# Kernel optimization log

Measured on AMD Instinct MI355X. Metric: run time of the kernel, lower is better.

The kernel has to match this reference:

```python
import jax, jax.numpy as jnp
import numpy as np

N, D, K, P, A = 16384, 256, 32, 64, 5
H, KD, NPT, FACT = 8, 32, 8, 2
RBF_BINS, RBF_MAX, REL_CLIP = 16, 10.0, 32


def _norm(v, eps=1e-6):
    return v * jax.lax.rsqrt(jnp.square(v).sum(-1, keepdims=True) + eps)


def extract_frames(pos):
    # pos: [N, A, 3]; backbone atoms 0=N, 1=CA, 2=C (Gram-Schmidt AF-style frame)
    n, ca, c = pos[:, 0], pos[:, 1], pos[:, 2]
    e1 = _norm(c - ca)
    u = n - ca
    e2 = _norm(u - (u * e1).sum(-1, keepdims=True) * e1)
    e3 = jnp.cross(e1, e2)
    R = jnp.stack([e1, e2, e3], axis=-1)  # [N,3,3], columns = frame axes
    t = ca
    local = jnp.einsum('nji,naj->nai', R, pos - t[:, None])  # R^T (p - t)
    return R, t, local


def distance_rbf(d):
    centers = jnp.linspace(0.0, RBF_MAX, RBF_BINS)
    sigma = RBF_MAX / RBF_BINS
    return jnp.exp(-jnp.square((d[..., None] - centers) / sigma))


def layer_norm(x, scale, offset, eps=1e-5):
    mu = x.mean(-1, keepdims=True)
    var = jnp.square(x - mu).mean(-1, keepdims=True)
    return (x - mu) * jax.lax.rsqrt(var + eps) * scale + offset


def setup_inputs() -> dict:
    key = jax.random.key(0)
    ks = jax.random.split(key, 20)
    f32 = jnp.float32
    rnd = lambda i, shape, s=0.02: jax.random.normal(ks[i], shape, f32) * s
    inp = {}
    inp['local'] = jax.random.normal(ks[0], (N, D), f32)
    inp['pos'] = jax.random.normal(ks[1], (N, A, 3), f32) * 3.0
    inp['neighbours'] = jax.random.randint(ks[2], (N, K), 0, N, jnp.int32)
    inp['resi'] = jnp.arange(N, dtype=jnp.int32) % 512
    inp['chain'] = jnp.arange(N, dtype=jnp.int32) // 2048
    inp['batch'] = jnp.arange(N, dtype=jnp.int32) // 4096
    inp['update_mask'] = jnp.ones((N, 1), bool)
    inp['mask'] = jnp.ones((N,), bool)
    FIN = A * 3 + A * RBF_BINS
    FPAIR = A * 3 + A * RBF_BINS + (2 * REL_CLIP + 1) + 2
    FOUT = H * KD + H * P + H * NPT * 3 + H * NPT
    inp['w_in'] = rnd(3, (FIN, D))
    inp['w_pair'] = rnd(4, (FPAIR, P))
    inp['b_pair'] = jnp.zeros((P,), f32)
    inp['ln1_s'] = jnp.ones((D,), f32); inp['ln1_o'] = jnp.zeros((D,), f32)
    inp['wq'] = rnd(5, (D, H * KD)); inp['wk'] = rnd(6, (D, H * KD)); inp['wv'] = rnd(7, (D, H * KD))
    inp['wqp'] = rnd(8, (D, H * NPT * 3)); inp['wkp'] = rnd(9, (D, H * NPT * 3)); inp['wvp'] = rnd(10, (D, H * NPT * 3))
    inp['wb'] = rnd(11, (P, H))
    inp['gamma'] = jnp.ones((H,), f32)
    inp['wo'] = rnd(12, (FOUT, D)); inp['bo'] = jnp.zeros((D,), f32)
    inp['ln2_s'] = jnp.ones((D,), f32); inp['ln2_o'] = jnp.zeros((D,), f32)
    DH = D * FACT
    inp['wg'] = rnd(13, (D, DH)); inp['wvm'] = rnd(14, (D, DH)); inp['wom'] = rnd(15, (DH, D))
    inp['ln3_s'] = jnp.ones((D,), f32); inp['ln3_o'] = jnp.zeros((D,), f32)
    inp['wpos'] = rnd(16, (D, A * 3))
    return inp


def reference(local, pos, w_in, w_pair, b_pair, ln1_s, ln1_o, wq, wk, wv, wqp, wkp, wvp,
              wb, gamma, wo, bo, ln2_s, ln2_o, wg, wvm, wom, ln3_s, ln3_o, wpos,
              neighbours, resi, chain, batch, update_mask, mask):
    n_res = local.shape[0]
    kk = neighbours.shape[1]
    R, t, local_pos = extract_frames(pos)  # [N,3,3], [N,3], [N,A,3]
    # --- geometric input features ---
    dloc = jnp.sqrt(jnp.square(local_pos).sum(-1) + 1e-12)
    feat = jnp.concatenate([_norm(local_pos).reshape(n_res, -1),
                            distance_rbf(dloc).reshape(n_res, -1)], axis=-1)
    local = local + feat @ w_in
    # --- pair features over kNN edges ---
    idx = jnp.clip(neighbours, 0, n_res - 1)
    pos_j = pos[idx]  # [N,K,A,3]
    rel = jnp.einsum('nji,nkaj->nkai', R, pos_j - t[:, None, None])  # neighbour atoms in frame i
    dij = jnp.sqrt(jnp.square(rel).sum(-1) + 1e-12)  # [N,K,A]
    dirs = rel / (dij[..., None] + 1e-6)
    rp = jnp.clip(resi[idx] - resi[:, None], -REL_CLIP, REL_CLIP) + REL_CLIP
    rp_oh = jax.nn.one_hot(rp, 2 * REL_CLIP + 1, dtype=local.dtype)
    same_chain = (chain[idx] == chain[:, None])[..., None].astype(local.dtype)
    same_batch = (batch[idx] == batch[:, None])[..., None].astype(local.dtype)
    pf = jnp.concatenate([dirs.reshape(n_res, kk, -1), distance_rbf(dij).reshape(n_res, kk, -1),
                          rp_oh, same_chain, same_batch], axis=-1)
    pair = jax.nn.gelu(pf @ w_pair + b_pair)  # [N,K,P]
    pair_mask = mask[:, None] & mask[idx] & (neighbours >= 0) & (batch[idx] == batch[:, None])
    # --- sparse invariant point attention ---
    x = layer_norm(local, ln1_s, ln1_o)
    q = (x @ wq).reshape(n_res, H, KD)
    k = (x @ wk).reshape(n_res, H, KD)
    v = (x @ wv).reshape(n_res, H, KD)
    to_glob = lambda pts: jnp.einsum('nij,nhpj->nhpi', R, pts) + t[:, None, None]
    qp = to_glob((x @ wqp).reshape(n_res, H, NPT, 3))
    kp = to_glob((x @ wkp).reshape(n_res, H, NPT, 3))
    vp = to_glob((x @ wvp).reshape(n_res, H, NPT, 3))
    qk = jnp.einsum('nhd,nkhd->nkh', q, k[idx]) / np.float32(np.sqrt(KD))
    d2 = jnp.square(qp[:, None] - kp[idx]).sum(-1).sum(-1)  # [N,K,H]
    wc = np.float32(np.sqrt(2.0 / (9.0 * NPT)))
    wl = np.float32(np.sqrt(1.0 / 3.0))
    logits = wl * (qk + pair @ wb - 0.5 * wc * jax.nn.softplus(gamma) * d2)
    logits = jnp.where(pair_mask[..., None], logits, -1e9)
    att = jax.nn.softmax(logits, axis=1)
    att = jnp.where(pair_mask[..., None], att, 0.0)
    o_s = jnp.einsum('nkh,nkhd->nhd', att, v[idx]).reshape(n_res, -1)
    o_pt = jnp.einsum('nkh,nkhpi->nhpi', att, vp[idx])
    o_pt = jnp.einsum('nji,nhpj->nhpi', R, o_pt - t[:, None, None])  # back to local frame
    o_n = jnp.sqrt(jnp.square(o_pt).sum(-1) + 1e-8)
    o_pr = jnp.einsum('nkh,nkc->nhc', att, pair).reshape(n_res, -1)
    ipa = jnp.concatenate([o_s, o_pr, o_pt.reshape(n_res, -1), o_n.reshape(n_res, -1)], -1) @ wo + bo
    local = local + ipa
    # --- gated MLP ---
    x = layer_norm(local, ln2_s, ln2_o)
    local = local + (jax.nn.gelu(x @ wg) * (x @ wvm)) @ wom
    # --- equivariant position update (scale = 1.0) ---
    x = layer_norm(local, ln3_s, ln3_o)
    new_lp = local_pos + (x @ wpos).reshape(n_res, A, 3)
    new_pos = jnp.einsum('nij,naj->nai', R, new_lp) + t[:, None]
    pos = jnp.where(update_mask[..., None], new_pos, pos)
    return local, pos
```

## Files before the change

kernel.cpp:

```cpp
#include <hip/hip_runtime.h>
#include <hip/hip_bf16.h>
#include <math.h>

#define DMODEL 256
#define KNB 32
#define NHEAD 8
#define FIN 95
#define FPD 95
#define KPAD 104
#define FOUT 1024
#define DHID 512
#define BTS 36
#define PRS 72

typedef __hip_bfloat16 bf16;
typedef __attribute__((ext_vector_type(8))) short short8;
typedef __attribute__((ext_vector_type(4))) float floatx4;

__device__ inline float B2F(bf16 x) { return __bfloat162float(x); }
__device__ inline bf16 F2B(float x) { return __float2bfloat16(x); }
__device__ inline unsigned short f2bs(float x) {
    bf16 h = __float2bfloat16(x);
    return *reinterpret_cast<unsigned short*>(&h);
}
__device__ inline float bs2f(short s) {
    return __uint_as_float(((unsigned)(unsigned short)s) << 16);
}

__device__ inline float gelu_f(float x) {
    float u = 1.5957691216057308f * x * (1.f + 0.044715f * x * x);
    float t = 1.f - 2.f / (1.f + __expf(u));
    return 0.5f * x * (1.f + t);
}

#define OFF_WALL 0
#define OFF_WO   344064
#define OFF_WG   606208
#define OFF_WVM  737280
#define OFF_WOM  868352
#define OFF_WP   999424
#define OFF_WIN  1006080
#define OFF_WBM  1032704
#define WT_TOTAL 1033728

__global__ __launch_bounds__(256) void kT(const float* __restrict__ wq, const float* __restrict__ wk,
                                          const float* __restrict__ wv, const float* __restrict__ wqp,
                                          const float* __restrict__ wkp, const float* __restrict__ wvp,
                                          const float* __restrict__ wo, const float* __restrict__ wg,
                                          const float* __restrict__ wvm, const float* __restrict__ wom,
                                          const float* __restrict__ w_pair, const float* __restrict__ w_in,
                                          const float* __restrict__ wbm,
                                          unsigned short* __restrict__ wt) {
    int stride = gridDim.x * 256;
    for (int e = blockIdx.x * 256 + threadIdx.x; e < WT_TOTAL; e += stride) {
        float v;
        if (e < OFF_WO) {
            int n = e >> 8, k = e & 255;
            if (n < 256) v = wq[k * 256 + n];
            else if (n < 512) v = wk[k * 256 + n - 256];
            else if (n < 768) v = wv[k * 256 + n - 512];
            else if (n < 960) v = wqp[k * 192 + n - 768];
            else if (n < 1152) v = wkp[k * 192 + n - 960];
            else v = wvp[k * 192 + n - 1152];
        } else if (e < OFF_WG) {
            int u = e - OFF_WO; int n = u >> 10, k = u & 1023;
            v = wo[k * 256 + n];
        } else if (e < OFF_WVM) {
            int u = e - OFF_WG; int n = u >> 8, k = u & 255;
            v = wg[k * 512 + n];
        } else if (e < OFF_WOM) {
            int u = e - OFF_WVM; int n = u >> 8, k = u & 255;
            v = wvm[k * 512 + n];
        } else if (e < OFF_WP) {
            int u = e - OFF_WOM; int n = u >> 9, k = u & 511;
            v = wom[k * 256 + n];
        } else if (e < OFF_WIN) {
            int u = e - OFF_WP; int n = u / KPAD, k = u % KPAD;
            v = (k < FPD) ? w_pair[k * 64 + n] : 0.f;
        } else if (e < OFF_WBM) {
            int u = e - OFF_WIN; int n = u / KPAD, k = u % KPAD;
            v = (k < FIN) ? w_in[k * 256 + n] : 0.f;
        } else {
            int u = e - OFF_WBM; int n = u >> 6, k = u & 63;
            v = (n < NHEAD) ? wbm[k * 8 + n] : 0.f;
        }
        wt[e] = f2bs(v);
    }
}

__global__ __launch_bounds__(256) void kA1(const float* __restrict__ pos,
                                           float* __restrict__ Rw,
                                           float* __restrict__ lpw,
                                           unsigned short* __restrict__ featb) {
    int tid = threadIdx.x;
    int res = tid >> 5, lt = tid & 31;
    int ri = blockIdx.x * 8 + res;
    const float* pp = pos + (size_t)ri * 15;
    float nx = pp[0], ny = pp[1], nz = pp[2];
    float cax = pp[3], cay = pp[4], caz = pp[5];
    float cx = pp[6], cy = pp[7], cz = pp[8];
    float e1x = cx - cax, e1y = cy - cay, e1z = cz - caz;
    float inv = rsqrtf(e1x * e1x + e1y * e1y + e1z * e1z + 1e-6f);
    e1x *= inv; e1y *= inv; e1z *= inv;
    float ux = nx - cax, uy = ny - cay, uz = nz - caz;
    float d = ux * e1x + uy * e1y + uz * e1z;
    float wx = ux - d * e1x, wy = uy - d * e1y, wz = uz - d * e1z;
    inv = rsqrtf(wx * wx + wy * wy + wz * wz + 1e-6f);
    float e2x = wx * inv, e2y = wy * inv, e2z = wz * inv;
    float e3x = e1y * e2z - e1z * e2y;
    float e3y = e1z * e2x - e1x * e2z;
    float e3z = e1x * e2y - e1y * e2x;
    float R[9] = {e1x, e2x, e3x, e1y, e2y, e3y, e1z, e2z, e3z};

    __shared__ float lpS[8][15];
    __shared__ float ddS[8][5], dinvS[8][5];

    if (lt < 9) Rw[(size_t)ri * 9 + lt] = R[lt];
    if (lt < 15) {
        int a = lt / 3, ii = lt % 3;
        float px = pp[a * 3 + 0] - cax, py = pp[a * 3 + 1] - cay, pz = pp[a * 3 + 2] - caz;
        float v = R[0 * 3 + ii] * px + R[1 * 3 + ii] * py + R[2 * 3 + ii] * pz;
        lpS[res][lt] = v;
        lpw[(size_t)ri * 15 + lt] = v;
    }
    __syncthreads();
    if (lt < 5) {
        float s = lpS[res][lt * 3] * lpS[res][lt * 3] + lpS[res][lt * 3 + 1] * lpS[res][lt * 3 + 1] +
                  lpS[res][lt * 3 + 2] * lpS[res][lt * 3 + 2];
        ddS[res][lt] = sqrtf(s + 1e-12f);
        dinvS[res][lt] = rsqrtf(s + 1e-6f);
    }
    __syncthreads();
    for (int e = lt; e < KPAD; e += 32) {
        float v;
        if (e < 15) v = lpS[res][e] * dinvS[res][e / 3];
        else if (e < 95) {
            int u = e - 15, a = u >> 4, b = u & 15;
            float z = (ddS[res][a] - (float)b * (10.f / 15.f)) * (1.f / 0.625f);
            v = __expf(-z * z);
        } else v = 0.f;
        featb[(size_t)ri * KPAD + e] = f2bs(v);
    }
}

__global__ __launch_bounds__(256) void kB(const float* __restrict__ local,
                                          const unsigned short* __restrict__ featb,
                                          const float* __restrict__ ln1_s,
                                          const float* __restrict__ ln1_o,
                                          const unsigned short* __restrict__ wAllT,
                                          const unsigned short* __restrict__ w_inT,
                                          float* __restrict__ dlocal,
                                          bf16* __restrict__ qbh, bf16* __restrict__ kvb,
                                          bf16* __restrict__ qpl, bf16* __restrict__ kpl,
                                          bf16* __restrict__ vpl) {
    int r0 = blockIdx.x * 32;
    int tid = threadIdx.x;
    __shared__ __align__(16) unsigned short featA[32 * KPAD];
    __shared__ __align__(16) unsigned short xbf[32 * 264];
    __shared__ float statsS[32 * 4];

    {
        const short8* src = reinterpret_cast<const short8*>(featb + (size_t)r0 * KPAD);
        short8* dst = reinterpret_cast<short8*>(featA);
        for (int c = tid; c < 32 * KPAD / 8; c += 256) dst[c] = src[c];
    }
    __syncthreads();

    int lane = tid & 63, w = tid >> 6;
    int mtile = w & 1, par = w >> 1;
    int m = lane & 15, quad = lane >> 4;

    short8 fa[3];
#pragma unroll
    for (int ks = 0; ks < 3; ks++)
        fa[ks] = *reinterpret_cast<const short8*>(&featA[(mtile * 16 + m) * KPAD + ks * 32 + quad * 8]);
    float lupv[8][4];
#pragma unroll
    for (int j = 0; j < 8; j++) {
        int nt = par + 2 * j;
        floatx4 c = {0.f, 0.f, 0.f, 0.f};
        const short8* bp = reinterpret_cast<const short8*>(w_inT + (size_t)(nt * 16 + m) * KPAD);
#pragma unroll
        for (int ks = 0; ks < 3; ks++)
            c = __builtin_amdgcn_mfma_f32_16x16x32_bf16(fa[ks], bp[ks * 4 + quad], c, 0, 0, 0);
        int col = nt * 16 + m;
#pragma unroll
        for (int r = 0; r < 4; r++) {
            int row = mtile * 16 + quad * 4 + r;
            float lv = local[(size_t)(r0 + row) * 256 + col] + c[r];
            lupv[j][r] = lv;
            dlocal[(size_t)(r0 + row) * 256 + col] = lv;
        }
    }
    {
        float s[4] = {0.f, 0.f, 0.f, 0.f}, ss[4] = {0.f, 0.f, 0.f, 0.f};
#pragma unroll
        for (int j = 0; j < 8; j++)
#pragma unroll
            for (int r = 0; r < 4; r++) { s[r] += lupv[j][r]; ss[r] += lupv[j][r] * lupv[j][r]; }
#pragma unroll
        for (int mask = 1; mask < 16; mask <<= 1)
#pragma unroll
            for (int r = 0; r < 4; r++) { s[r] += __shfl_xor(s[r], mask); ss[r] += __shfl_xor(ss[r], mask); }
        if (m == 0) {
#pragma unroll
            for (int r = 0; r < 4; r++) {
                int row = mtile * 16 + quad * 4 + r;
                statsS[row * 4 + par * 2 + 0] = s[r];
                statsS[row * 4 + par * 2 + 1] = ss[r];
            }
        }
    }
    __syncthreads();
    {
        float mu[4], rs_[4];
#pragma unroll
        for (int r = 0; r < 4; r++) {
            int row = mtile * 16 + quad * 4 + r;
            float S = statsS[row * 4 + 0] + statsS[row * 4 + 2];
            float SS = statsS[row * 4 + 1] + statsS[row * 4 + 3];
            float m_ = S * (1.f / 256.f);
            mu[r] = m_;
            rs_[r] = rsqrtf(SS * (1.f / 256.f) - m_ * m_ + 1e-5f);
        }
#pragma unroll
        for (int j = 0; j < 8; j++) {
            int col = (par + 2 * j) * 16 + m;
            float g = ln1_s[col], o = ln1_o[col];
#pragma unroll
            for (int r = 0; r < 4; r++) {
                int row = mtile * 16 + quad * 4 + r;
                xbf[row * 264 + col] = f2bs((lupv[j][r] - mu[r]) * rs_[r] * g + o);
            }
        }
    }
    __syncthreads();

    short8 afr[8];
#pragma unroll
    for (int ks = 0; ks < 8; ks++)
        afr[ks] = *reinterpret_cast<const short8*>(&xbf[(mtile * 16 + m) * 264 + ks * 32 + quad * 8]);
    for (int nt = par; nt < 84; nt += 2) {
        floatx4 c = {0.f, 0.f, 0.f, 0.f};
        const short8* bp = reinterpret_cast<const short8*>(wAllT + (size_t)(nt * 16 + m) * 256);
#pragma unroll
        for (int ks = 0; ks < 8; ks++)
            c = __builtin_amdgcn_mfma_f32_16x16x32_bf16(afr[ks], bp[ks * 4 + quad], c, 0, 0, 0);
        int colg = nt * 16 + m;
        bf16* O; int c0, ncol;
        if (colg < 256)       { O = qbh; c0 = colg;        ncol = 256; }
        else if (colg < 768)  { O = kvb; c0 = colg - 256;  ncol = 512; }
        else if (colg < 960)  { O = qpl; c0 = colg - 768;  ncol = 192; }
        else if (colg < 1152) { O = kpl; c0 = colg - 960;  ncol = 192; }
        else                  { O = vpl; c0 = colg - 1152; ncol = 192; }
#pragma unroll
        for (int r = 0; r < 4; r++) {
            int rg = r0 + mtile * 16 + quad * 4 + r;
            O[(size_t)rg * ncol + c0] = F2B(c[r]);
        }
    }
}

__global__ __launch_bounds__(256) void kP(const bf16* __restrict__ qpl,
                                          const bf16* __restrict__ kpl,
                                          const bf16* __restrict__ vpl,
                                          const float* __restrict__ Rw,
                                          const float* __restrict__ pos,
                                          float* __restrict__ qpg,
                                          bf16* __restrict__ kvpgh) {
    int r0 = blockIdx.x * 4;
    int tid = threadIdx.x;
    for (int u = tid; u < 4 * 192; u += 256) {
        int r = u / 192, e = u % 192, hp = e / 3, ii = e % 3;
        int ri = r0 + r;
        float R0 = Rw[(size_t)ri * 9 + ii * 3 + 0];
        float R1 = Rw[(size_t)ri * 9 + ii * 3 + 1];
        float R2 = Rw[(size_t)ri * 9 + ii * 3 + 2];
        float tt = pos[(size_t)ri * 15 + 3 + ii];
        size_t base = (size_t)ri * 192 + hp * 3;
        qpg[(size_t)ri * 192 + e] = R0 * B2F(qpl[base]) + R1 * B2F(qpl[base + 1]) + R2 * B2F(qpl[base + 2]) + tt;
        kvpgh[(size_t)ri * 384 + e] = F2B(R0 * B2F(kpl[base]) + R1 * B2F(kpl[base + 1]) + R2 * B2F(kpl[base + 2]));
        kvpgh[(size_t)ri * 384 + 192 + e] = F2B(R0 * B2F(vpl[base]) + R1 * B2F(vpl[base + 1]) + R2 * B2F(vpl[base + 2]));
    }
}

__global__ __launch_bounds__(256, 4) void kC(const float* __restrict__ pos,
                                          const int* __restrict__ nbr,
                                          const int* __restrict__ resi,
                                          const int* __restrict__ chain,
                                          const int* __restrict__ batch,
                                          const int* __restrict__ mask,
                                          const float* __restrict__ Rw,
                                          const float* __restrict__ w_pair,
                                          const unsigned short* __restrict__ wT,
                                          const float* __restrict__ b_pair,
                                          const unsigned short* __restrict__ wbmT,
                                          const float* __restrict__ gamma,
                                          const bf16* __restrict__ qbh,
                                          const bf16* __restrict__ kvb,
                                          const float* __restrict__ qpg,
                                          const bf16* __restrict__ kvpgh,
                                          bf16* __restrict__ ipab,
                                          int N) {
    int i = blockIdx.x;
    int tid = threadIdx.x;
    __shared__ __align__(16) unsigned short BigT[256 * BTS];
    __shared__ __align__(16) unsigned short pairR[32 * PRS];
    __shared__ __align__(16) unsigned short attb[16 * 40];
    __shared__ __align__(16) float qS[256];
    __shared__ __align__(16) float qpS[192];
    __shared__ __align__(16) float pbS[256];
    __shared__ float spS[NHEAD];
    __shared__ float tjS[KNB][3];
    __shared__ float attjS[24];
    __shared__ int idxS[KNB], rpS[KNB], scS[KNB], sbS[KNB], pmS[KNB];
    __shared__ __align__(16) union UShare {
        unsigned short pfA[32 * KPAD];
        struct { float ipaS[FOUT]; float optg[192]; } o;
    } uS;

    int kk_s = tid & 31, seg = tid >> 5;
    int jpre;
    {
        int nb = nbr[(size_t)i * KNB + kk_s];
        jpre = min(max(nb, 0), N - 1);
    }
    short8 pv0, pv1, pv2, pv3, pp0, pp1, pp2;
    {
        const short8* vsrc = reinterpret_cast<const short8*>(kvb + (size_t)jpre * 512 + 256 + seg * 32);
        pv0 = vsrc[0]; pv1 = vsrc[1]; pv2 = vsrc[2]; pv3 = vsrc[3];
        const unsigned short* vpb = reinterpret_cast<const unsigned short*>(kvpgh) + (size_t)jpre * 384 + 192 + seg * 24;
        const short8* vpsrc = reinterpret_cast<const short8*>(vpb);
        pp0 = vpsrc[0]; pp1 = vpsrc[1]; pp2 = vpsrc[2];
    }

    float R[9];
#pragma unroll
    for (int u = 0; u < 9; u++) R[u] = Rw[(size_t)i * 9 + u];
    float t0 = pos[(size_t)i * 15 + 3];
    float t1 = pos[(size_t)i * 15 + 4];
    float t2 = pos[(size_t)i * 15 + 5];

    qS[tid] = B2F(qbh[(size_t)i * 256 + tid]);
    if (tid < 192) qpS[tid] = qpg[(size_t)i * 192 + tid];
    if (tid < NHEAD) spS[tid] = log1pf(__expf(gamma[tid]));
    if (tid < KNB) {
        int nb = nbr[(size_t)i * KNB + tid];
        int j = min(max(nb, 0), N - 1);
        idxS[tid] = j;
        int rp = resi[j] - resi[i];
        rp = min(max(rp, -32), 32) + 32;
        rpS[tid] = rp;
        scS[tid] = (chain[j] == chain[i]) ? 1 : 0;
        sbS[tid] = (batch[j] == batch[i]) ? 1 : 0;
        pmS[tid] = (mask[i] != 0 && mask[j] != 0 && nb >= 0 && batch[j] == batch[i]) ? 1 : 0;
    }
    __syncthreads();
    if (tid < 160) {
        int kk = tid & 31, a = tid >> 5;
        int j = idxS[kk];
        const float* pj = pos + (size_t)j * 15 + a * 3;
        float pj0 = pj[0], pj1 = pj[1], pj2 = pj[2];
        if (a == 1) { tjS[kk][0] = pj0; tjS[kk][1] = pj1; tjS[kk][2] = pj2; }
        float px = pj0 - t0, py = pj1 - t1, pz = pj2 - t2;
        float r0_ = R[0] * px + R[3] * py + R[6] * pz;
        float r1_ = R[1] * px + R[4] * py + R[7] * pz;
        float r2_ = R[2] * px + R[5] * py + R[8] * pz;
        float s = r0_ * r0_ + r1_ * r1_ + r2_ * r2_;
        float dij = sqrtf(s + 1e-12f);
        float di = 1.f / (dij + 1e-6f);
        uS.pfA[kk * KPAD + a * 3 + 0] = f2bs(r0_ * di);
        uS.pfA[kk * KPAD + a * 3 + 1] = f2bs(r1_ * di);
        uS.pfA[kk * KPAD + a * 3 + 2] = f2bs(r2_ * di);
        for (int b = 0; b < 16; b++) {
            float z = (dij - (float)b * (10.f / 15.f)) * (1.f / 0.625f);
            uS.pfA[kk * KPAD + 15 + a * 16 + b] = f2bs(__expf(-z * z));
        }
    }
    if (tid < KNB) uS.pfA[tid * KPAD + FPD] = 0;
    __syncthreads();

    {
        int lane = tid & 63;
        int wv = tid >> 6;
        int n0 = wv * 16;
        int mrow = lane & 15;
        int quad = lane >> 4;
        floatx4 c0 = {0.f, 0.f, 0.f, 0.f};
        floatx4 c1 = {0.f, 0.f, 0.f, 0.f};
#pragma unroll
        for (int ks = 0; ks < 3; ks++) {
            int k0 = ks * 32 + quad * 8;
            short8 a0 = *reinterpret_cast<const short8*>(&uS.pfA[mrow * KPAD + k0]);
            short8 a1 = *reinterpret_cast<const short8*>(&uS.pfA[(16 + mrow) * KPAD + k0]);
            short8 bb = *reinterpret_cast<const short8*>(&wT[(n0 + mrow) * KPAD + k0]);
            c0 = __builtin_amdgcn_mfma_f32_16x16x32_bf16(a0, bb, c0, 0, 0, 0);
            c1 = __builtin_amdgcn_mfma_f32_16x16x32_bf16(a1, bb, c1, 0, 0, 0);
        }
        int col = n0 + mrow;
        float bp = b_pair[col];
        float w160 = w_pair[160 * 64 + col];
        float w161 = w_pair[161 * 64 + col];
#pragma unroll
        for (int mt = 0; mt < 2; mt++) {
            floatx4 cc = mt ? c1 : c0;
#pragma unroll
            for (int r = 0; r < 4; r++) {
                int row = mt * 16 + quad * 4 + r;
                float s = cc[r] + bp + w_pair[(95 + rpS[row]) * 64 + col] +
                          (scS[row] ? w160 : 0.f) + (sbS[row] ? w161 : 0.f);
                pairR[row * PRS + col] = f2bs(gelu_f(s));
            }
        }
    }
    __syncthreads();

    short8 pk0, pk1, pk2, pk3, pq0, pq1, pq2;
    {
        int kk2 = tid >> 3, h2 = tid & 7;
        int j2 = idxS[kk2];
        const short8* ksrc = reinterpret_cast<const short8*>(kvb + (size_t)j2 * 512 + h2 * 32);
        pk0 = ksrc[0]; pk1 = ksrc[1]; pk2 = ksrc[2]; pk3 = ksrc[3];
        const unsigned short* kpb = reinterpret_cast<const unsigned short*>(kvpgh) + (size_t)j2 * 384 + h2 * 24;
        const short8* kpsrc = reinterpret_cast<const short8*>(kpb);
        pq0 = kpsrc[0]; pq1 = kpsrc[1]; pq2 = kpsrc[2];
    }
    {
        int kk = kk_s;
#pragma unroll
        for (int c = 0; c < 8; c++) BigT[(seg * 32 + c) * BTS + kk] = (unsigned short)pv0[c];
#pragma unroll
        for (int c = 0; c < 8; c++) BigT[(seg * 32 + 8 + c) * BTS + kk] = (unsigned short)pv1[c];
#pragma unroll
        for (int c = 0; c < 8; c++) BigT[(seg * 32 + 16 + c) * BTS + kk] = (unsigned short)pv2[c];
#pragma unroll
        for (int c = 0; c < 8; c++) BigT[(seg * 32 + 24 + c) * BTS + kk] = (unsigned short)pv3[c];
    }
    {
        int w = tid >> 6;
        if (w < 2) {
            int lane = tid & 63, la = lane & 15, quad = lane >> 4;
            floatx4 c = {0.f, 0.f, 0.f, 0.f};
#pragma unroll
            for (int ks = 0; ks < 2; ks++) {
                short8 a = *reinterpret_cast<const short8*>(&pairR[(w * 16 + la) * PRS + ks * 32 + quad * 8]);
                short8 b = *reinterpret_cast<const short8*>(wbmT + la * 64 + ks * 32 + quad * 8);
                c = __builtin_amdgcn_mfma_f32_16x16x32_bf16(a, b, c, 0, 0, 0);
            }
            if (la < NHEAD) {
#pragma unroll
                for (int r = 0; r < 4; r++)
                    pbS[(w * 16 + quad * 4 + r) * 8 + la] = c[r];
            }
        }
    }
    __syncthreads();

    {
        int kk = tid >> 3, h = tid & 7;
        float qk = 0.f;
        const floatx4* qh4 = reinterpret_cast<const floatx4*>(qS + h * 32);
        short8 kvv[4] = {pk0, pk1, pk2, pk3};
#pragma unroll
        for (int e = 0; e < 4; e++) {
            short8 kv = kvv[e];
            floatx4 qa = qh4[2 * e], qb = qh4[2 * e + 1];
            qk += qa[0] * bs2f(kv[0]) + qa[1] * bs2f(kv[1]) + qa[2] * bs2f(kv[2]) + qa[3] * bs2f(kv[3]) +
                  qb[0] * bs2f(kv[4]) + qb[1] * bs2f(kv[5]) + qb[2] * bs2f(kv[6]) + qb[3] * bs2f(kv[7]);
        }
        qk *= 0.17677669529663687f;
        float d2 = 0.f;
        const float* qp = qpS + h * 24;
        float tj[3] = {tjS[kk][0], tjS[kk][1], tjS[kk][2]};
        short8 kpv[3] = {pq0, pq1, pq2};
#pragma unroll
        for (int e8 = 0; e8 < 3; e8++)
#pragma unroll
            for (int c8 = 0; c8 < 8; c8++) {
                int x = e8 * 8 + c8;
                float df = (qp[x] - tj[x % 3]) - bs2f(kpv[e8][c8]);
                d2 += df * df;
            }
        float pb = pbS[kk * 8 + h];
        float lgt = 0.5773502691896258f * (qk + pb - (1.f / 12.f) * spS[h] * d2);
        pbS[kk * 8 + h] = pmS[kk] ? lgt : -1e9f;
    }
    __syncthreads();

    if (tid < 64) {
        int h = tid >> 3, sub = tid & 7;
        float m = -INFINITY;
        float lv[4];
#pragma unroll
        for (int q = 0; q < 4; q++) {
            lv[q] = pbS[(sub + 8 * q) * 8 + h];
            m = fmaxf(m, lv[q]);
        }
#pragma unroll
        for (int mk = 1; mk < 8; mk <<= 1) m = fmaxf(m, __shfl_xor(m, mk));
        float s = 0.f, ex[4];
#pragma unroll
        for (int q = 0; q < 4; q++) { ex[q] = __expf(lv[q] - m); s += ex[q]; }
#pragma unroll
        for (int mk = 1; mk < 8; mk <<= 1) s += __shfl_xor(s, mk);
        float invs = 1.f / s;
#pragma unroll
        for (int q = 0; q < 4; q++) {
            int kk = sub + 8 * q;
            float a = pmS[kk] ? ex[q] * invs : 0.f;
            attb[h * 40 + kk] = f2bs(a);
            pbS[kk * 8 + h] = a;
        }
    } else if (tid < 128) {
        int t2 = tid - 64;
        int h2 = 8 + (t2 >> 3);
        int k0 = (t2 & 7) * 4;
#pragma unroll
        for (int q = 0; q < 4; q++) attb[h2 * 40 + k0 + q] = 0;
    }
    __syncthreads();

    int la_ = (tid & 63) & 15, quad_ = (tid & 63) >> 4, w_ = tid >> 6;
    short8 af = *reinterpret_cast<const short8*>(&attb[la_ * 40 + quad_ * 8]);
    float* oB = uS.o.ipaS;

#pragma unroll
    for (int n4 = 0; n4 < 4; n4++) {
        int colg = (w_ * 4 + n4) * 16 + la_;
        union { short8 s; unsigned long long u[2]; } bb;
        const unsigned long long* bp = reinterpret_cast<const unsigned long long*>(&BigT[colg * BTS + quad_ * 8]);
        bb.u[0] = bp[0]; bb.u[1] = bp[1];
        floatx4 z = {0.f, 0.f, 0.f, 0.f};
        floatx4 d = __builtin_amdgcn_mfma_f32_16x16x32_bf16(af, bb.s, z, 0, 0, 0);
        int h_req = colg >> 5;
        if (quad_ == (h_req >> 2)) {
#pragma unroll
            for (int r = 0; r < 4; r++)
                if ((h_req & 3) == r) oB[(h_req << 5) + (colg & 31)] = d[r];
        }
    }
    if (tid < 24) {
        int h = tid / 3, c = tid % 3;
        float s = 0.f;
#pragma unroll
        for (int kk = 0; kk < KNB; kk++) s += pbS[kk * 8 + h] * tjS[kk][c];
        attjS[tid] = s;
    }
    __syncthreads();

    {
        int kk = kk_s;
#pragma unroll
        for (int c = 0; c < 8; c++) BigT[(seg * 24 + c) * BTS + kk] = (unsigned short)pp0[c];
#pragma unroll
        for (int c = 0; c < 8; c++) BigT[(seg * 24 + 8 + c) * BTS + kk] = (unsigned short)pp1[c];
#pragma unroll
        for (int c = 0; c < 8; c++) BigT[(seg * 24 + 16 + c) * BTS + kk] = (unsigned short)pp2[c];
    }
#pragma unroll
    for (int q = 0; q < 8; q++) {
        int u = tid + q * 256;
        int row = u & 31, col = u >> 5;
        BigT[(192 + col) * BTS + row] = pairR[row * PRS + col];
    }
    __syncthreads();

#pragma unroll
    for (int n4 = 0; n4 < 4; n4++) {
        int colg = (w_ * 4 + n4) * 16 + la_;
        union { short8 s; unsigned long long u[2]; } bb;
        const unsigned long long* bp = reinterpret_cast<const unsigned long long*>(&BigT[colg * BTS + quad_ * 8]);
        bb.u[0] = bp[0]; bb.u[1] = bp[1];
        floatx4 z = {0.f, 0.f, 0.f, 0.f};
        floatx4 d = __builtin_amdgcn_mfma_f32_16x16x32_bf16(af, bb.s, z, 0, 0, 0);
        if (colg < 192) {
            int h_req = colg / 24;
            if (quad_ == (h_req >> 2)) {
#pragma unroll
                for (int r = 0; r < 4; r++)
                    if ((h_req & 3) == r) oB[1024 + colg] = d[r];
            }
        } else if (quad_ < 2) {
            int c = colg - 192;
#pragma unroll
            for (int r = 0; r < 4; r++)
                oB[256 + (quad_ * 4 + r) * 64 + c] = d[r];
        }
    }
    __syncthreads();

    if (tid < 192) {
        int hp = tid / 3, ii = tid % 3;
        int h = hp >> 3;
        const float* optg = uS.o.ipaS + 1024;
        float v0 = optg[hp * 3 + 0] + attjS[h * 3 + 0] - t0;
        float v1 = optg[hp * 3 + 1] + attjS[h * 3 + 1] - t1;
        float v2 = optg[hp * 3 + 2] + attjS[h * 3 + 2] - t2;
        uS.o.ipaS[768 + tid] = R[0 + ii] * v0 + R[3 + ii] * v1 + R[6 + ii] * v2;
    }
    __syncthreads();
    if (tid < 64) {
        float a0 = uS.o.ipaS[768 + tid * 3], a1 = uS.o.ipaS[768 + tid * 3 + 1], a2 = uS.o.ipaS[768 + tid * 3 + 2];
        uS.o.ipaS[960 + tid] = sqrtf(a0 * a0 + a1 * a1 + a2 * a2 + 1e-8f);
    }
    __syncthreads();
    for (int u = tid; u < FOUT; u += 256) ipab[(size_t)i * FOUT + u] = F2B(uS.o.ipaS[u]);
}

__global__ __launch_bounds__(256) void kDE(const bf16* __restrict__ ipab,
                                           const unsigned short* __restrict__ woT,
                                           const float* __restrict__ bo,
                                           const float* __restrict__ ln2_s,
                                           const float* __restrict__ ln2_o,
                                           const unsigned short* __restrict__ wgT,
                                           const unsigned short* __restrict__ wvmT,
                                           const unsigned short* __restrict__ womT,
                                           float* __restrict__ dlocal) {
    int r0 = blockIdx.x * 32;
    int tid = threadIdx.x;
    __shared__ __align__(16) unsigned short xbf[32 * 264];
    __shared__ __align__(16) unsigned short hbf[32 * 520];
    __shared__ float statsS[32 * 4];
    int lane = tid & 63, w = tid >> 6;
    int mtile = w & 1, par = w >> 1, m = lane & 15, quad = lane >> 4;

    floatx4 l2[8];
#pragma unroll
    for (int j = 0; j < 8; j++) l2[j] = {0.f, 0.f, 0.f, 0.f};
    const short8* arow = reinterpret_cast<const short8*>(ipab + (size_t)(r0 + mtile * 16 + m) * 1024);
    for (int ks = 0; ks < 32; ks++) {
        short8 a = arow[ks * 4 + quad];
#pragma unroll
        for (int j = 0; j < 8; j++) {
            int nt = par + 2 * j;
            const short8* bp = reinterpret_cast<const short8*>(woT + (size_t)(nt * 16 + m) * 1024);
            l2[j] = __builtin_amdgcn_mfma_f32_16x16x32_bf16(a, bp[ks * 4 + quad], l2[j], 0, 0, 0);
        }
    }
#pragma unroll
    for (int j = 0; j < 8; j++) {
        int colg = (par + 2 * j) * 16 + m;
        float bov = bo[colg];
#pragma unroll
        for (int r = 0; r < 4; r++) {
            int row = mtile * 16 + quad * 4 + r;
            l2[j][r] += dlocal[(size_t)(r0 + row) * 256 + colg] + bov;
        }
    }
    {
        float s[4] = {0.f, 0.f, 0.f, 0.f}, ss[4] = {0.f, 0.f, 0.f, 0.f};
#pragma unroll
        for (int j = 0; j < 8; j++)
#pragma unroll
            for (int r = 0; r < 4; r++) { s[r] += l2[j][r]; ss[r] += l2[j][r] * l2[j][r]; }
#pragma unroll
        for (int mask = 1; mask < 16; mask <<= 1)
#pragma unroll
            for (int r = 0; r < 4; r++) { s[r] += __shfl_xor(s[r], mask); ss[r] += __shfl_xor(ss[r], mask); }
        if (m == 0) {
#pragma unroll
            for (int r = 0; r < 4; r++) {
                int row = mtile * 16 + quad * 4 + r;
                statsS[row * 4 + par * 2 + 0] = s[r];
                statsS[row * 4 + par * 2 + 1] = ss[r];
            }
        }
    }
    __syncthreads();
    {
        float mu[4], rs_[4];
#pragma unroll
        for (int r = 0; r < 4; r++) {
            int row = mtile * 16 + quad * 4 + r;
            float S = statsS[row * 4 + 0] + statsS[row * 4 + 2];
            float SS = statsS[row * 4 + 1] + statsS[row * 4 + 3];
            float m_ = S * (1.f / 256.f);
            mu[r] = m_;
            rs_[r] = rsqrtf(SS * (1.f / 256.f) - m_ * m_ + 1e-5f);
        }
#pragma unroll
        for (int j = 0; j < 8; j++) {
            int colg = (par + 2 * j) * 16 + m;
            float g = ln2_s[colg], o = ln2_o[colg];
#pragma unroll
            for (int r = 0; r < 4; r++) {
                int row = mtile * 16 + quad * 4 + r;
                xbf[row * 264 + colg] = f2bs((l2[j][r] - mu[r]) * rs_[r] * g + o);
            }
        }
    }
    __syncthreads();
    short8 afr[8];
#pragma unroll
    for (int ks = 0; ks < 8; ks++)
        afr[ks] = *reinterpret_cast<const short8*>(&xbf[(mtile * 16 + m) * 264 + ks * 32 + quad * 8]);
    for (int nt = par; nt < 32; nt += 2) {
        floatx4 cg = {0.f, 0.f, 0.f, 0.f};
        floatx4 cv = {0.f, 0.f, 0.f, 0.f};
        const short8* bg = reinterpret_cast<const short8*>(wgT + (size_t)(nt * 16 + m) * 256);
        const short8* bv = reinterpret_cast<const short8*>(wvmT + (size_t)(nt * 16 + m) * 256);
#pragma unroll
        for (int ks = 0; ks < 8; ks++) {
            cg = __builtin_amdgcn_mfma_f32_16x16x32_bf16(afr[ks], bg[ks * 4 + quad], cg, 0, 0, 0);
            cv = __builtin_amdgcn_mfma_f32_16x16x32_bf16(afr[ks], bv[ks * 4 + quad], cv, 0, 0, 0);
        }
#pragma unroll
        for (int r = 0; r < 4; r++) {
            int row = mtile * 16 + quad * 4 + r;
            hbf[row * 520 + nt * 16 + m] = f2bs(gelu_f(cg[r]) * cv[r]);
        }
    }
    __syncthreads();
    floatx4 acc[8];
#pragma unroll
    for (int j = 0; j < 8; j++) acc[j] = {0.f, 0.f, 0.f, 0.f};
    for (int ks = 0; ks < 16; ks++) {
        short8 a = *reinterpret_cast<const short8*>(&hbf[(mtile * 16 + m) * 520 + ks * 32 + quad * 8]);
#pragma unroll
        for (int j = 0; j < 8; j++) {
            int nt = par + 2 * j;
            const short8* bp = reinterpret_cast<const short8*>(womT + (size_t)(nt * 16 + m) * 512);
            acc[j] = __builtin_amdgcn_mfma_f32_16x16x32_bf16(a, bp[ks * 4 + quad], acc[j], 0, 0, 0);
        }
    }
#pragma unroll
    for (int j = 0; j < 8; j++) {
        int colg = (par + 2 * j) * 16 + m;
#pragma unroll
        for (int r = 0; r < 4; r++) {
            int row = mtile * 16 + quad * 4 + r;
            dlocal[(size_t)(r0 + row) * 256 + colg] = l2[j][r] + acc[j][r];
        }
    }
}

__global__ __launch_bounds__(256) void kF(const float* __restrict__ dlocal,
                                          const float* __restrict__ ln3_s,
                                          const float* __restrict__ ln3_o,
                                          const float* __restrict__ wpos,
                                          const float* __restrict__ lpw,
                                          const float* __restrict__ Rw,
                                          const float* __restrict__ pos,
                                          const int* __restrict__ umask,
                                          float* __restrict__ outp) {
    int tid = threadIdx.x;
    int r = tid >> 5, lt = tid & 31;
    int ri = blockIdx.x * 8 + r;
    __shared__ float x3S[8][256];
    __shared__ float nlS[8][15];
    {
        const floatx4* src = reinterpret_cast<const floatx4*>(dlocal + (size_t)ri * 256 + lt * 8);
        floatx4 v0 = src[0], v1 = src[1];
        float s = 0.f, ss = 0.f;
#pragma unroll
        for (int q = 0; q < 4; q++) {
            s += v0[q] + v1[q];
            ss += v0[q] * v0[q] + v1[q] * v1[q];
        }
#pragma unroll
        for (int mask = 1; mask < 32; mask <<= 1) { s += __shfl_xor(s, mask); ss += __shfl_xor(ss, mask); }
        float mu = s * (1.f / 256.f);
        float var = ss * (1.f / 256.f) - mu * mu;
        float rs = rsqrtf(var + 1e-5f);
#pragma unroll
        for (int q = 0; q < 4; q++) {
            int f0 = lt * 8 + q, f1 = lt * 8 + 4 + q;
            x3S[r][f0] = (v0[q] - mu) * rs * ln3_s[f0] + ln3_o[f0];
            x3S[r][f1] = (v1[q] - mu) * rs * ln3_s[f1] + ln3_o[f1];
        }
    }
    __syncthreads();
    {
        int g = tid >> 5, sub = tid & 31;
        for (int out = g; out < 120; out += 8) {
            int rr = out / 15, e = out % 15;
            float partial = 0.f;
#pragma unroll
            for (int i2 = 0; i2 < 8; i2++) {
                int f = sub + 32 * i2;
                partial += x3S[rr][f] * wpos[f * 15 + e];
            }
#pragma unroll
            for (int mask = 1; mask < 32; mask <<= 1) partial += __shfl_xor(partial, mask);
            if (sub == 0) nlS[rr][e] = lpw[(size_t)(blockIdx.x * 8 + rr) * 15 + e] + partial;
        }
    }
    __syncthreads();
    if (tid < 120) {
        int rr = tid / 15, e = tid % 15;
        int rj = blockIdx.x * 8 + rr;
        int a2 = e / 3, ii = e % 3;
        float R0 = Rw[(size_t)rj * 9 + ii * 3 + 0];
        float R1 = Rw[(size_t)rj * 9 + ii * 3 + 1];
        float R2 = Rw[(size_t)rj * 9 + ii * 3 + 2];
        float tt = pos[(size_t)rj * 15 + 3 + ii];
        float np = R0 * nlS[rr][a2 * 3 + 0] + R1 * nlS[rr][a2 * 3 + 1] + R2 * nlS[rr][a2 * 3 + 2] + tt;
        float old = pos[(size_t)rj * 15 + e];
        outp[(size_t)rj * 15 + e] = (umask[rj] != 0) ? np : old;
    }
}

extern "C" void kernel_launch(void* const* d_in, const int* in_sizes, int n_in,
                              void* d_out, int out_size, void* d_ws, size_t ws_size,
                              hipStream_t stream) {
    static const int map_dict[31] = {0, 1, 2, 3, 4, 5, 6, 7, 8, 9, 10, 11, 12, 13, 14, 15,
                                     16, 17, 18, 19, 20, 21, 22, 23, 24, 25, 26, 27, 28, 29, 30};
    static const int map_sig[31] = {0, 1, 25, 26, 27, 28, 29, 30, 2, 3, 4, 5, 6, 7, 8, 9,
                                    10, 11, 12, 13, 14, 15, 16, 17, 18, 19, 20, 21, 22, 23, 24};
    const int* M = (in_sizes[2] == FIN * DMODEL) ? map_sig : map_dict;

    const float* local = (const float*)d_in[M[0]];
    const float* pos = (const float*)d_in[M[1]];
    const int* nbr = (const int*)d_in[M[2]];
    const int* resi = (const int*)d_in[M[3]];
    const int* chain = (const int*)d_in[M[4]];
    const int* batch = (const int*)d_in[M[5]];
    const int* umask = (const int*)d_in[M[6]];
    const int* mask = (const int*)d_in[M[7]];
    const float* w_in = (const float*)d_in[M[8]];
    const float* w_pair = (const float*)d_in[M[9]];
    const float* b_pair = (const float*)d_in[M[10]];
    const float* ln1_s = (const float*)d_in[M[11]];
    const float* ln1_o = (const float*)d_in[M[12]];
    const float* wq = (const float*)d_in[M[13]];
    const float* wk = (const float*)d_in[M[14]];
    const float* wv = (const float*)d_in[M[15]];
    const float* wqp = (const float*)d_in[M[16]];
    const float* wkp = (const float*)d_in[M[17]];
    const float* wvp = (const float*)d_in[M[18]];
    const float* wbm = (const float*)d_in[M[19]];
    const float* gamma = (const float*)d_in[M[20]];
    const float* wo = (const float*)d_in[M[21]];
    const float* bo = (const float*)d_in[M[22]];
    const float* ln2_s = (const float*)d_in[M[23]];
    const float* ln2_o = (const float*)d_in[M[24]];
    const float* wg = (const float*)d_in[M[25]];
    const float* wvm = (const float*)d_in[M[26]];
    const float* wom = (const float*)d_in[M[27]];
    const float* ln3_s = (const float*)d_in[M[28]];
    const float* ln3_o = (const float*)d_in[M[29]];
    const float* wpos = (const float*)d_in[M[30]];

    int N = in_sizes[0] / DMODEL;

    float* out_local = (float*)d_out;
    float* out_pos = out_local + (size_t)N * DMODEL;

    char* wsb = (char*)d_ws;
    float* Rw = (float*)wsb;   wsb += (size_t)N * 9 * 4;
    float* lpw = (float*)wsb;  wsb += (size_t)N * 15 * 4;
    bf16* qbh = (bf16*)wsb;    wsb += (size_t)N * 256 * 2;
    bf16* kvb = (bf16*)wsb;    wsb += (size_t)N * 512 * 2;
    bf16* qpl = (bf16*)wsb;    wsb += (size_t)N * 192 * 2;
    bf16* kpl = (bf16*)wsb;    wsb += (size_t)N * 192 * 2;
    bf16* vpl = (bf16*)wsb;    wsb += (size_t)N * 192 * 2;
    bf16* ipab = (bf16*)wsb;   wsb += (size_t)N * 1024 * 2;
    float* qpg = (float*)wsb;  wsb += (size_t)N * 192 * 4;
    bf16* kvpgh = (bf16*)wsb;  wsb += (size_t)N * 384 * 2;
    unsigned short* featb = (unsigned short*)wsb; wsb += (size_t)N * KPAD * 2;
    unsigned short* wtrans = (unsigned short*)wsb; wsb += (size_t)WT_TOTAL * 2;
    unsigned short* wAllT = wtrans + OFF_WALL;
    unsigned short* woT   = wtrans + OFF_WO;
    unsigned short* wgT   = wtrans + OFF_WG;
    unsigned short* wvmT  = wtrans + OFF_WVM;
    unsigned short* womT  = wtrans + OFF_WOM;
    unsigned short* wpT   = wtrans + OFF_WP;
    unsigned short* winT  = wtrans + OFF_WIN;
    unsigned short* wbmT  = wtrans + OFF_WBM;

    dim3 blk(256);
    hipLaunchKernelGGL(kT, dim3(512), blk, 0, stream, wq, wk, wv, wqp, wkp, wvp,
                       wo, wg, wvm, wom, w_pair, w_in, wbm, wtrans);
    hipLaunchKernelGGL(kA1, dim3(N / 8), blk, 0, stream, pos, Rw, lpw, featb);
    hipLaunchKernelGGL(kB, dim3(N / 32), blk, 0, stream, local, featb, ln1_s, ln1_o, wAllT, winT,
                       out_local, qbh, kvb, qpl, kpl, vpl);
    hipLaunchKernelGGL(kP, dim3(N / 4), blk, 0, stream, qpl, kpl, vpl, Rw, pos, qpg, kvpgh);
    hipLaunchKernelGGL(kC, dim3(N), blk, 0, stream, pos, nbr, resi, chain, batch, mask, Rw,
                       w_pair, wpT, b_pair, wbmT, gamma, qbh, kvb, qpg, kvpgh, ipab, N);
    hipLaunchKernelGGL(kDE, dim3(N / 32), blk, 0, stream, ipab, woT, bo, ln2_s, ln2_o,
                       wgT, wvmT, womT, out_local);
    hipLaunchKernelGGL(kF, dim3(N / 8), blk, 0, stream, out_local, ln3_s, ln3_o, wpos, lpw, Rw, pos,
                       umask, out_pos);
}
```

Measured before the change: 638.8 us.

## Merge weight transpose into frame kernel, split kB columns across two blocks

The weight-transpose kernel and the frame/feature kernel become one launch, with extra blocks handling the transpose, which removes a launch boundary. kB now uses twice as many blocks, each computing half of the 84 output column tiles. Only the half-0 block writes dlocal, while both halves redo the w_in projection and layernorm, trading duplicated work for more parallelism. kC also gets a different pairR transpose indexing, an optg buffer in the union, and a redundant qk loop whose result is immediately discarded.

After: 649.5 us. Within noise of the previous version (+1.7%).

```diff
diff --git a/kernel.cpp b/kernel.cpp
--- a/kernel.cpp
+++ b/kernel.cpp
@@ -42,57 +42,61 @@
 #define OFF_WIN  1006080
 #define OFF_WBM  1032704
 #define WT_TOTAL 1033728
-
-__global__ __launch_bounds__(256) void kT(const float* __restrict__ wq, const float* __restrict__ wk,
-                                          const float* __restrict__ wv, const float* __restrict__ wqp,
-                                          const float* __restrict__ wkp, const float* __restrict__ wvp,
-                                          const float* __restrict__ wo, const float* __restrict__ wg,
-                                          const float* __restrict__ wvm, const float* __restrict__ wom,
-                                          const float* __restrict__ w_pair, const float* __restrict__ w_in,
-                                          const float* __restrict__ wbm,
-                                          unsigned short* __restrict__ wt) {
-    int stride = gridDim.x * 256;
-    for (int e = blockIdx.x * 256 + threadIdx.x; e < WT_TOTAL; e += stride) {
-        float v;
-        if (e < OFF_WO) {
-            int n = e >> 8, k = e & 255;
-            if (n < 256) v = wq[k * 256 + n];
-            else if (n < 512) v = wk[k * 256 + n - 256];
-            else if (n < 768) v = wv[k * 256 + n - 512];
-            else if (n < 960) v = wqp[k * 192 + n - 768];
-            else if (n < 1152) v = wkp[k * 192 + n - 960];
-            else v = wvp[k * 192 + n - 1152];
-        } else if (e < OFF_WG) {
-            int u = e - OFF_WO; int n = u >> 10, k = u & 1023;
-            v = wo[k * 256 + n];
-        } else if (e < OFF_WVM) {
-            int u = e - OFF_WG; int n = u >> 8, k = u & 255;
-            v = wg[k * 512 + n];
-        } else if (e < OFF_WOM) {
-            int u = e - OFF_WVM; int n = u >> 8, k = u & 255;
-            v = wvm[k * 512 + n];
-        } else if (e < OFF_WP) {
-            int u = e - OFF_WOM; int n = u >> 9, k = u & 511;
-            v = wom[k * 256 + n];
-        } else if (e < OFF_WIN) {
-            int u = e - OFF_WP; int n = u / KPAD, k = u % KPAD;
-            v = (k < FPD) ? w_pair[k * 64 + n] : 0.f;
-        } else if (e < OFF_WBM) {
-            int u = e - OFF_WIN; int n = u / KPAD, k = u % KPAD;
-            v = (k < FIN) ? w_in[k * 256 + n] : 0.f;
-        } else {
-            int u = e - OFF_WBM; int n = u >> 6, k = u & 63;
-            v = (n < NHEAD) ? wbm[k * 8 + n] : 0.f;
-        }
-        wt[e] = f2bs(v);
-    }
-}
-
-__global__ __launch_bounds__(256) void kA1(const float* __restrict__ pos,
+#define KT_BLOCKS 512
+
+__global__ __launch_bounds__(256) void kTA(const float* __restrict__ wq, const float* __restrict__ wk,
+                                           const float* __restrict__ wv, const float* __restrict__ wqp,
+                                           const float* __restrict__ wkp, const float* __restrict__ wvp,
+                                           const float* __restrict__ wo, const float* __restrict__ wg,
+                                           const float* __restrict__ wvm, const float* __restrict__ wom,
+                                           const float* __restrict__ w_pair, const float* __restrict__ w_in,
+                                           const float* __restrict__ wbm,
+                                           unsigned short* __restrict__ wt,
+                                           const float* __restrict__ pos,
                                            float* __restrict__ Rw,
                                            float* __restrict__ lpw,
-                                           unsigned short* __restrict__ featb) {
+                                           unsigned short* __restrict__ featb,
+                                           int nA1) {
     int tid = threadIdx.x;
+    if ((int)blockIdx.x >= nA1) {
+        int kblk = blockIdx.x - nA1;
+        int stride = KT_BLOCKS * 256;
+        for (int e = kblk * 256 + tid; e < WT_TOTAL; e += stride) {
+            float v;
+            if (e < OFF_WO) {
+                int n = e >> 8, k = e & 255;
+                if (n < 256) v = wq[k * 256 + n];
+                else if (n < 512) v = wk[k * 256 + n - 256];
+                else if (n < 768) v = wv[k * 256 + n - 512];
+                else if (n < 960) v = wqp[k * 192 + n - 768];
+                else if (n < 1152) v = wkp[k * 192 + n - 960];
+                else v = wvp[k * 192 + n - 1152];
+            } else if (e < OFF_WG) {
+                int u = e - OFF_WO; int n = u >> 10, k = u & 1023;
+                v = wo[k * 256 + n];
+            } else if (e < OFF_WVM) {
+                int u = e - OFF_WG; int n = u >> 8, k = u & 255;
+                v = wg[k * 512 + n];
+            } else if (e < OFF_WOM) {
+                int u = e - OFF_WVM; int n = u >> 8, k = u & 255;
+                v = wvm[k * 512 + n];
+            } else if (e < OFF_WP) {
+                int u = e - OFF_WOM; int n = u >> 9, k = u & 511;
+                v = wom[k * 256 + n];
+            } else if (e < OFF_WIN) {
+                int u = e - OFF_WP; int n = u / KPAD, k = u % KPAD;
+                v = (k < FPD) ? w_pair[k * 64 + n] : 0.f;
+            } else if (e < OFF_WBM) {
+                int u = e - OFF_WIN; int n = u / KPAD, k = u % KPAD;
+                v = (k < FIN) ? w_in[k * 256 + n] : 0.f;
+            } else {
+                int u = e - OFF_WBM; int n = u >> 6, k = u & 63;
+                v = (n < NHEAD) ? wbm[k * 8 + n] : 0.f;
+            }
+            wt[e] = f2bs(v);
+        }
+        return;
+    }
     int res = tid >> 5, lt = tid & 31;
     int ri = blockIdx.x * 8 + res;
     const float* pp = pos + (size_t)ri * 15;
@@ -153,7 +157,8 @@
                                           bf16* __restrict__ qbh, bf16* __restrict__ kvb,
                                           bf16* __restrict__ qpl, bf16* __restrict__ kpl,
                                           bf16* __restrict__ vpl) {
-    int r0 = blockIdx.x * 32;
+    int r0 = (blockIdx.x >> 1) * 32;
+    int half = blockIdx.x & 1;
     int tid = threadIdx.x;
     __shared__ __align__(16) unsigned short featA[32 * KPAD];
     __shared__ __align__(16) unsigned short xbf[32 * 264];
@@ -189,7 +194,7 @@
             int row = mtile * 16 + quad * 4 + r;
             float lv = local[(size_t)(r0 + row) * 256 + col] + c[r];
             lupv[j][r] = lv;
-            dlocal[(size_t)(r0 + row) * 256 + col] = lv;
+            if (half == 0) dlocal[(size_t)(r0 + row) * 256 + col] = lv;
         }
     }
     {
@@ -240,7 +245,8 @@
 #pragma unroll
     for (int ks = 0; ks < 8; ks++)
         afr[ks] = *reinterpret_cast<const short8*>(&xbf[(mtile * 16 + m) * 264 + ks * 32 + quad * 8]);
-    for (int nt = par; nt < 84; nt += 2) {
+    int ntEnd = 42 * (half + 1);
+    for (int nt = 42 * half + par; nt < ntEnd; nt += 2) {
         floatx4 c = {0.f, 0.f, 0.f, 0.f};
         const short8* bp = reinterpret_cast<const short8*>(wAllT + (size_t)(nt * 16 + m) * 256);
 #pragma unroll
@@ -466,6 +472,14 @@
             short8 kv = kvv[e];
             floatx4 qa = qh4[2 * e], qb = qh4[2 * e + 1];
             qk += qa[0] * bs2f(kv[0]) + qa[1] * bs2f(kv[1]) + qa[2] * bs2f(kv[2]) + qa[3] * bs2f(kv[3]) +
+                  qb[0] * bs2f(kv[4]) + qb[1] * bs2f(kv[5]) + qb[2] * bs2f(kv[6]) + qb[7 - 7] * 0.f;
+        }
+        qk = 0.f;
+#pragma unroll
+        for (int e = 0; e < 4; e++) {
+            short8 kv = kvv[e];
+            floatx4 qa = qh4[2 * e], qb = qh4[2 * e + 1];
+            qk += qa[0] * bs2f(kv[0]) + qa[1] * bs2f(kv[1]) + qa[2] * bs2f(kv[2]) + qa[3] * bs2f(kv[3]) +
                   qb[0] * bs2f(kv[4]) + qb[1] * bs2f(kv[5]) + qb[2] * bs2f(kv[6]) + qb[3] * bs2f(kv[7]);
         }
         qk *= 0.17677669529663687f;
@@ -522,7 +536,6 @@
 
     int la_ = (tid & 63) & 15, quad_ = (tid & 63) >> 4, w_ = tid >> 6;
     short8 af = *reinterpret_cast<const short8*>(&attb[la_ * 40 + quad_ * 8]);
-    float* oB = uS.o.ipaS;
 
 #pragma unroll
     for (int n4 = 0; n4 < 4; n4++) {
@@ -536,7 +549,7 @@
         if (quad_ == (h_req >> 2)) {
 #pragma unroll
             for (int r = 0; r < 4; r++)
-                if ((h_req & 3) == r) oB[(h_req << 5) + (colg & 31)] = d[r];
+                if ((h_req & 3) == r) uS.o.ipaS[(h_req << 5) + (colg & 31)] = d[r];
         }
     }
     if (tid < 24) {
@@ -559,8 +572,8 @@
     }
 #pragma unroll
     for (int q = 0; q < 8; q++) {
-        int u = tid + q * 256;
-        int row = u & 31, col = u >> 5;
+        int row = tid >> 3;
+        int col = (tid & 7) + q * 8;
         BigT[(192 + col) * BTS + row] = pairR[row * PRS + col];
     }
     __syncthreads();
@@ -578,13 +591,13 @@
             if (quad_ == (h_req >> 2)) {
 #pragma unroll
                 for (int r = 0; r < 4; r++)
-                    if ((h_req & 3) == r) oB[1024 + colg] = d[r];
+                    if ((h_req & 3) == r) uS.o.optg[colg] = d[r];
             }
         } else if (quad_ < 2) {
             int c = colg - 192;
 #pragma unroll
             for (int r = 0; r < 4; r++)
-                oB[256 + (quad_ * 4 + r) * 64 + c] = d[r];
+                uS.o.ipaS[256 + (quad_ * 4 + r) * 64 + c] = d[r];
         }
     }
     __syncthreads();
@@ -592,10 +605,9 @@
     if (tid < 192) {
         int hp = tid / 3, ii = tid % 3;
         int h = hp >> 3;
-        const float* optg = uS.o.ipaS + 1024;
-        float v0 = optg[hp * 3 + 0] + attjS[h * 3 + 0] - t0;
-        float v1 = optg[hp * 3 + 1] + attjS[h * 3 + 1] - t1;
-        float v2 = optg[hp * 3 + 2] + attjS[h * 3 + 2] - t2;
+        float v0 = uS.o.optg[hp * 3 + 0] + attjS[h * 3 + 0] - t0;
+        float v1 = uS.o.optg[hp * 3 + 1] + attjS[h * 3 + 1] - t1;
+        float v2 = uS.o.optg[hp * 3 + 2] + attjS[h * 3 + 2] - t2;
         uS.o.ipaS[768 + tid] = R[0 + ii] * v0 + R[3 + ii] * v1 + R[6 + ii] * v2;
     }
     __syncthreads();
@@ -868,11 +880,11 @@
     unsigned short* winT  = wtrans + OFF_WIN;
     unsigned short* wbmT  = wtrans + OFF_WBM;
 
+    int nA1 = N / 8;
     dim3 blk(256);
-    hipLaunchKernelGGL(kT, dim3(512), blk, 0, stream, wq, wk, wv, wqp, wkp, wvp,
-                       wo, wg, wvm, wom, w_pair, w_in, wbm, wtrans);
-    hipLaunchKernelGGL(kA1, dim3(N / 8), blk, 0, stream, pos, Rw, lpw, featb);
-    hipLaunchKernelGGL(kB, dim3(N / 32), blk, 0, stream, local, featb, ln1_s, ln1_o, wAllT, winT,
+    hipLaunchKernelGGL(kTA, dim3(nA1 + KT_BLOCKS), blk, 0, stream, wq, wk, wv, wqp, wkp, wvp,
+                       wo, wg, wvm, wom, w_pair, w_in, wbm, wtrans, pos, Rw, lpw, featb, nA1);
+    hipLaunchKernelGGL(kB, dim3(N / 16), blk, 0, stream, local, featb, ln1_s, ln1_o, wAllT, winT,
                        out_local, qbh, kvb, qpl, kpl, vpl);
     hipLaunchKernelGGL(kP, dim3(N / 4), blk, 0, stream, qpl, kpl, vpl, Rw, pos, qpg, kvpgh);
     hipLaunchKernelGGL(kC, dim3(N), blk, 0, stream, pos, nbr, resi, chain, batch, mask, Rw,
```
